# Optimization experiments

Measured on AMD Instinct MI355X. Metric: run time of the kernel, lower is better.

The kernel has to match this reference:

```python
import jax, jax.numpy as jnp
import numpy as np

V = 5023          # FLAME vertex count
NJ = 5            # joints: global, neck, jaw, eyeL, eyeR
N_SHAPE = 100
N_EXP = 50
PARENTS = np.array([-1, 0, 1, 1, 1], dtype=np.int64)  # static kintree
N_BATCH = 2048


def setup_inputs() -> dict:
    key = jax.random.key(0)
    ks = jax.random.split(key, 12)
    N = N_BATCH
    shape = jax.random.normal(ks[0], (N, N_SHAPE), jnp.float32)
    exp = jax.random.normal(ks[1], (N, N_EXP), jnp.float32)
    neck_pose = 0.1 * jax.random.normal(ks[2], (N, 3), jnp.float32)
    jaw_pose = 0.1 * jax.random.normal(ks[3], (N, 3), jnp.float32)
    eye_pose = 0.1 * jax.random.normal(ks[4], (N, 6), jnp.float32)
    v_template = jax.random.normal(ks[5], (V, 3), jnp.float32)
    shapedirs = 0.01 * jax.random.normal(ks[6], (V, 3, N_SHAPE + N_EXP), jnp.float32)
    posedirs = 0.01 * jax.random.normal(ks[7], (36, V * 3), jnp.float32)
    J_regressor = jax.random.uniform(ks[8], (NJ, V), jnp.float32)
    J_regressor = J_regressor / J_regressor.sum(axis=1, keepdims=True)
    lbs_weights = jax.random.uniform(ks[9], (V, NJ), jnp.float32)
    lbs_weights = lbs_weights / lbs_weights.sum(axis=1, keepdims=True)
    parents = jnp.asarray(PARENTS)
    return dict(shape=shape, exp=exp, neck_pose=neck_pose, jaw_pose=jaw_pose,
                eye_pose=eye_pose, v_template=v_template, shapedirs=shapedirs,
                posedirs=posedirs, J_regressor=J_regressor, lbs_weights=lbs_weights,
                parents=parents)


def rodrigues(rot_vecs):
    """Axis-angle [...,3] -> rotation matrices [...,3,3] (matches SMPL/FLAME impl)."""
    angle = jnp.linalg.norm(rot_vecs + 1e-8, axis=-1, keepdims=True)
    rd = rot_vecs / angle
    cos = jnp.cos(angle)[..., None]
    sin = jnp.sin(angle)[..., None]
    rx, ry, rz = rd[..., 0], rd[..., 1], rd[..., 2]
    z = jnp.zeros_like(rx)
    K = jnp.stack([z, -rz, ry, rz, z, -rx, -ry, rx, z], axis=-1).reshape(rd.shape + (3,))
    I = jnp.eye(3, dtype=rot_vecs.dtype)
    return I + sin * K + (1.0 - cos) * (K @ K)


def flame_forward(shape, exp, neck_pose, jaw_pose, eye_pose, v_template,
                  shapedirs, posedirs, J_regressor, lbs_weights):
    N = shape.shape[0]
    dt = shape.dtype
    betas = jnp.concatenate([shape, exp], axis=1)                      # [N,150]
    # full pose: zeroed global rot + neck + jaw + eyes -> [N,NJ,3]
    full_pose = jnp.concatenate([jnp.zeros_like(jaw_pose), neck_pose,
                                 jaw_pose, eye_pose], axis=1).reshape(N, NJ, 3)
    # shape blendshapes
    v_shaped = v_template[None] + jnp.einsum('bl,vkl->bvk', betas, shapedirs)  # [N,V,3]
    J = jnp.einsum('jv,bvk->bjk', J_regressor, v_shaped)               # [N,NJ,3]
    # pose blendshapes
    R = rodrigues(full_pose)                                           # [N,NJ,3,3]
    pose_feature = (R[:, 1:] - jnp.eye(3, dtype=dt)).reshape(N, (NJ - 1) * 9)
    v_posed = v_shaped + (pose_feature @ posedirs).reshape(N, V, 3)
    # kinematic chain (static 5-joint tree)
    rel_J = J.at[:, 1:].add(-J[:, PARENTS[1:]])
    Rt = jnp.concatenate([R, rel_J[..., None]], axis=-1)               # [N,NJ,3,4]
    bottom = jnp.broadcast_to(jnp.array([0., 0., 0., 1.], dtype=dt), (N, NJ, 1, 4))
    T = jnp.concatenate([Rt, bottom], axis=2)                          # [N,NJ,4,4]
    chain = [T[:, 0]]
    for i in range(1, NJ):
        chain.append(chain[int(PARENTS[i])] @ T[:, i])
    G = jnp.stack(chain, axis=1)                                       # [N,NJ,4,4]
    # remove rest-pose joint locations from the transforms
    J_h = jnp.concatenate([J, jnp.zeros((N, NJ, 1), dt)], axis=-1)     # [N,NJ,4]
    t_corr = jnp.einsum('bjrc,bjc->bjr', G, J_h)
    A = G.at[..., 3].add(-t_corr)                                      # [N,NJ,4,4]
    # linear blend skinning
    Tw = jnp.einsum('vj,bjrc->bvrc', lbs_weights, A)                   # [N,V,4,4]
    v_h = jnp.concatenate([v_posed, jnp.ones((N, V, 1), dt)], axis=-1)
    verts = jnp.einsum('bvrc,bvc->bvr', Tw, v_h)[..., :3]              # [N,V,3]
    return verts


def reference(shape, exp, neck_pose, jaw_pose, eye_pose, v_template,
              shapedirs, posedirs, J_regressor, lbs_weights, parents):
    # parents is a static buffer (PARENTS) -- accepted for signature parity.
    return flame_forward(shape, exp, neck_pose, jaw_pose, eye_pose, v_template,
                         shapedirs, posedirs, J_regressor, lbs_weights)
```

## Files before the change

kernel.cpp:

```cpp
#include <hip/hip_runtime.h>
#include <hip/hip_bf16.h>
#include <math.h>

#define NV   5023
#define N3   15069
#define NB   2048
#define NTIL 79
#define NPAD (NTIL*192)

#define WS_JD_B   0
#define WS_ATR_B  9216
#define WS_AB_B   795648
#define WS_BB_B   1582080

#define GP_J 126
#define GP_S 1067
#define GP_P 237

typedef __attribute__((ext_vector_type(8))) short short8;
typedef __attribute__((ext_vector_type(4))) float floatx4;

static __device__ __forceinline__ unsigned short f2bf(float x) {
    union { __hip_bfloat16 h; unsigned short s; } u;
    u.h = __float2bfloat16(x);
    return u.s;
}
static __device__ __forceinline__ unsigned int pk2(float a, float b) {
    return (unsigned int)f2bf(a) | ((unsigned int)f2bf(b) << 16);
}

#define BAR_LGKM() do { \
    asm volatile("s_waitcnt lgkmcnt(0)" ::: "memory"); \
    __builtin_amdgcn_s_barrier(); \
    asm volatile("" ::: "memory"); \
} while (0)

__global__ void k_prep(const float* __restrict__ Jreg,
                       const float* __restrict__ sdirs,
                       const float* __restrict__ vt,
                       const float* __restrict__ pdirs,
                       char* __restrict__ ws) {
    __shared__ float JregL[200];
    __shared__ float PL[36][65];
    const int t = threadIdx.x;

    if (blockIdx.x < GP_J) {
        int slice = blockIdx.x;
        int start = slice * 40;
        int end   = min(start + 40, NV);
        if (t < 200) {
            int j = t / 40, vl = t % 40;
            int v = start + vl;
            JregL[t] = (v < NV) ? Jreg[j * NV + v] : 0.f;
        }
        __syncthreads();
        int s0 = t, s1 = t + 256;
        float a0[5] = {0,0,0,0,0}, a1[5] = {0,0,0,0,0};
        #pragma unroll 2
        for (int v = start; v < end; ++v) {
            int vl = v - start;
            float x0 = (s0 < 450) ? sdirs[(size_t)v * 450 + s0]
                     : (s0 < 453 ? vt[v * 3 + (s0 - 450)] : 0.f);
            float x1 = (s1 < 450) ? sdirs[(size_t)v * 450 + s1]
                     : (s1 < 453 ? vt[v * 3 + (s1 - 450)] : 0.f);
            #pragma unroll
            for (int j = 0; j < 5; ++j) {
                float w = JregL[j * 40 + vl];
                a0[j] += w * x0; a1[j] += w * x1;
            }
        }
        float* Jd = (float*)(ws + WS_JD_B);
        #pragma unroll
        for (int j = 0; j < 5; ++j) {
            if (s0 < 453) atomicAdd(&Jd[j * 453 + s0], a0[j]);
            if (s1 < 453) atomicAdd(&Jd[j * 453 + s1], a1[j]);
        }
    } else if (blockIdx.x < GP_J + GP_S) {
        int idx = (blockIdx.x - GP_J) * 256 + t;
        if (idx < NPAD * 18) {
            int n = idx / 18, g = idx % 18;
            __hip_bfloat16* dst = (__hip_bfloat16*)(ws + WS_BB_B) + (size_t)n * 192 + g * 8;
            if (n < N3) {
                const float* src = sdirs + (size_t)n * 150 + g * 8;
                float2 p0 = *(const float2*)(src);
                float2 p1 = *(const float2*)(src + 2);
                float2 p2 = *(const float2*)(src + 4);
                float2 p3 = *(const float2*)(src + 6);
                unsigned int w[4] = { pk2(p0.x, p0.y), pk2(p1.x, p1.y),
                                      pk2(p2.x, p2.y), pk2(p3.x, p3.y) };
                *(int4*)dst = *(int4*)w;
            } else {
                int4 z = {0, 0, 0, 0};
                *(int4*)dst = z;
            }
        }
    } else {
        int pb = blockIdx.x - (GP_J + GP_S);
        int n0 = pb * 64;
        #pragma unroll
        for (int j = 0; j < 9; ++j) {
            int flat = j * 256 + t;
            int k = flat >> 6, i = flat & 63;
            int n = n0 + i;
            PL[k][i] = (n < N3) ? pdirs[(size_t)k * N3 + n] : 0.f;
        }
        __syncthreads();
        #pragma unroll
        for (int j = 0; j < 2; ++j) {
            int idx2 = j * 256 + t;
            if (idx2 < 384) {
                int r = idx2 / 6, g = idx2 % 6;
                int n = n0 + r;
                int k0 = 144 + g * 8;
                __hip_bfloat16 val[8];
                #pragma unroll
                for (int e = 0; e < 8; ++e) {
                    int k = k0 + e;
                    float v = 0.f;
                    if (k < 150)      v = (n < N3) ? sdirs[(size_t)n * 150 + k] : 0.f;
                    else if (k < 186) v = PL[k - 150][r];
                    val[e] = __float2bfloat16(v);
                }
                *(int4*)((__hip_bfloat16*)(ws + WS_BB_B) + (size_t)n * 192 + k0) = *(int4*)val;
            }
        }
    }
}

__global__ void k_batch(const float* __restrict__ shp,
                        const float* __restrict__ expn,
                        const float* __restrict__ neck,
                        const float* __restrict__ jaw,
                        const float* __restrict__ eye,
                        char* __restrict__ ws) {
    __shared__ float JdL[2265];
    {
        const float* Jd = (const float*)(ws + WS_JD_B);
        for (int i = threadIdx.x; i < 2265; i += 64) JdL[i] = Jd[i];
    }
    __syncthreads();
    int b = blockIdx.x * 64 + threadIdx.x;
    float* Atr = (float*)(ws + WS_ATR_B) + (size_t)b * 60;
    unsigned int* A32 = (unsigned int*)((char*)ws + WS_AB_B + (size_t)b * 384);

    float J[15];
    #pragma unroll
    for (int jk = 0; jk < 15; ++jk) J[jk] = JdL[(jk / 3) * 453 + 450 + (jk % 3)];

    for (int l4 = 0; l4 < 25; ++l4) {
        float4 be = *(const float4*)(shp + (size_t)b * 100 + l4 * 4);
        A32[2*l4]     = pk2(be.x, be.y);
        A32[2*l4 + 1] = pk2(be.z, be.w);
        float bev[4] = {be.x, be.y, be.z, be.w};
        #pragma unroll
        for (int e = 0; e < 4; ++e) {
            int l = l4 * 4 + e;
            #pragma unroll
            for (int jj = 0; jj < 5; ++jj)
                #pragma unroll
                for (int kk = 0; kk < 3; ++kk)
                    J[jj * 3 + kk] += JdL[jj * 453 + kk * 150 + l] * bev[e];
        }
    }
    for (int l2 = 0; l2 < 25; ++l2) {
        float2 be = *(const float2*)(expn + (size_t)b * 50 + l2 * 2);
        A32[50 + l2] = pk2(be.x, be.y);
        float bev[2] = {be.x, be.y};
        #pragma unroll
        for (int e = 0; e < 2; ++e) {
            int l = 100 + l2 * 2 + e;
            #pragma unroll
            for (int jj = 0; jj < 5; ++jj)
                #pragma unroll
                for (int kk = 0; kk < 3; ++kk)
                    J[jj * 3 + kk] += JdL[jj * 453 + kk * 150 + l] * bev[e];
        }
    }

    float R[5][9];
    for (int jj = 0; jj < 5; ++jj) {
        float rx, ry, rz;
        if (jj == 0)      { rx = 0.f; ry = 0.f; rz = 0.f; }
        else if (jj == 1) { rx = neck[b*3]; ry = neck[b*3+1]; rz = neck[b*3+2]; }
        else if (jj == 2) { rx = jaw[b*3];  ry = jaw[b*3+1];  rz = jaw[b*3+2];  }
        else if (jj == 3) { rx = eye[b*6];  ry = eye[b*6+1];  rz = eye[b*6+2];  }
        else              { rx = eye[b*6+3]; ry = eye[b*6+4]; rz = eye[b*6+5];  }
        float ax = rx + 1e-8f, ay = ry + 1e-8f, az = rz + 1e-8f;
        float angle = sqrtf(ax*ax + ay*ay + az*az);
        float inv = 1.f / angle;
        float ux = rx * inv, uy = ry * inv, uz = rz * inv;
        float c = cosf(angle), s = sinf(angle);
        float K[9] = {0.f, -uz, uy,  uz, 0.f, -ux,  -uy, ux, 0.f};
        float KK[9];
        #pragma unroll
        for (int r = 0; r < 3; ++r)
            #pragma unroll
            for (int cc = 0; cc < 3; ++cc) {
                float a = 0.f;
                #pragma unroll
                for (int m = 0; m < 3; ++m) a += K[r*3+m] * K[m*3+cc];
                KK[r*3+cc] = a;
            }
        #pragma unroll
        for (int e = 0; e < 9; ++e) R[jj][e] = s * K[e] + (1.f - c) * KK[e];
        R[jj][0] += 1.f; R[jj][4] += 1.f; R[jj][8] += 1.f;
    }

    float pf_loc[36];
    #pragma unroll
    for (int jj = 1; jj < 5; ++jj)
        #pragma unroll
        for (int e = 0; e < 9; ++e)
            pf_loc[(jj-1)*9 + e] = R[jj][e] - ((e == 0 || e == 4 || e == 8) ? 1.f : 0.f);
    #pragma unroll
    for (int i = 0; i < 18; ++i) A32[75 + i] = pk2(pf_loc[2*i], pf_loc[2*i + 1]);
    A32[93] = 0u; A32[94] = 0u; A32[95] = 0u;

    float G[5][12];
    #pragma unroll
    for (int r = 0; r < 3; ++r) {
        #pragma unroll
        for (int cc = 0; cc < 3; ++cc) G[0][r*4+cc] = R[0][r*3+cc];
        G[0][r*4+3] = J[r];
    }
    const int par[5] = {-1, 0, 1, 1, 1};
    for (int jj = 1; jj < 5; ++jj) {
        int p = par[jj];
        float rel[3];
        #pragma unroll
        for (int r = 0; r < 3; ++r) rel[r] = J[jj*3+r] - J[p*3+r];
        #pragma unroll
        for (int r = 0; r < 3; ++r) {
            #pragma unroll
            for (int cc = 0; cc < 3; ++cc) {
                float a = 0.f;
                #pragma unroll
                for (int m = 0; m < 3; ++m) a += G[p][r*4+m] * R[jj][m*3+cc];
                G[jj][r*4+cc] = a;
            }
            float tt = G[p][r*4+3];
            #pragma unroll
            for (int m = 0; m < 3; ++m) tt += G[p][r*4+m] * rel[m];
            G[jj][r*4+3] = tt;
        }
    }
    for (int jj = 0; jj < 5; ++jj)
        #pragma unroll
        for (int r = 0; r < 3; ++r) {
            float tc = 0.f;
            #pragma unroll
            for (int m = 0; m < 3; ++m) tc += G[jj][r*4+m] * J[jj*3+m];
            Atr[jj*12 + r*4 + 0] = G[jj][r*4+0];
            Atr[jj*12 + r*4 + 1] = G[jj][r*4+1];
            Atr[jj*12 + r*4 + 2] = G[jj][r*4+2];
            Atr[jj*12 + r*4 + 3] = G[jj][r*4+3] - tc;
        }
}

#define A_OFF  0
#define B_OFF  8704
#define S_VT   33
#define S_AT   61
#define VT_T_OFF 0
#define ATR_OFF  25344
#define VTQ_OFF  33152
#define LBS_OFF  33920
#define SMEM_BYTES 35200

__global__ __launch_bounds__(256, 3) void k_mega(
        const char* __restrict__ ws,
        const float* __restrict__ vt,
        const float* __restrict__ lbsw,
        float* __restrict__ out) {
    __shared__ __align__(16) unsigned char smem[SMEM_BYTES];
    const unsigned char* AbG = (const unsigned char*)ws + WS_AB_B;
    const unsigned char* BbG = (const unsigned char*)ws + WS_BB_B;
    const float* AtrG = (const float*)(ws + WS_ATR_B);

    const int ntile = blockIdx.y;
    const int b0    = blockIdx.x * 64;
    const int t     = threadIdx.x;
    const int lane  = t & 63;
    const int wn    = t >> 6;
    const int l15 = lane & 15, quad = lane >> 4;

    floatx4 acc[4][3];
    #pragma unroll
    for (int f = 0; f < 4; ++f)
        #pragma unroll
        for (int g = 0; g < 3; ++g) {
            floatx4 z = {0.f, 0.f, 0.f, 0.f};
            acc[f][g] = z;
        }

    for (int chunk = 0; chunk < 3; ++chunk) {
        __syncthreads();
        #pragma unroll
        for (int i = 0; i < 2; ++i) {
            int flat = i * 256 + t;
            int row = flat >> 3, piece = flat & 7;
            *(float4*)(smem + A_OFF + row * 136 + piece * 16) =
                *(const float4*)(AbG + (size_t)(b0 + row) * 384 + chunk * 128 + piece * 16);
        }
        #pragma unroll
        for (int i = 0; i < 6; ++i) {
            int flat = i * 256 + t;
            int row = flat >> 3, piece = flat & 7;
            *(float4*)(smem + B_OFF + row * 136 + piece * 16) =
                *(const float4*)(BbG + (size_t)(ntile * 192 + row) * 384 + chunk * 128 + piece * 16);
        }
        __syncthreads();
        #pragma unroll
        for (int ks = 0; ks < 2; ++ks) {
            short8 af[4];
            #pragma unroll
            for (int f = 0; f < 4; ++f)
                af[f] = *(const short8*)(smem + A_OFF + (f * 16 + l15) * 136 + ks * 64 + quad * 16);
            #pragma unroll
            for (int g = 0; g < 3; ++g) {
                short8 bf = *(const short8*)(smem + B_OFF + (wn * 48 + g * 16 + l15) * 136 + ks * 64 + quad * 16);
                #pragma unroll
                for (int f = 0; f < 4; ++f)
                    acc[f][g] = __builtin_amdgcn_mfma_f32_16x16x32_bf16(af[f], bf, acc[f][g], 0, 0, 0);
            }
        }
    }
    __syncthreads();

    float* vtT  = (float*)(smem + VT_T_OFF);
    float* atrS = (float*)(smem + ATR_OFF);
    float* vtQ  = (float*)(smem + VTQ_OFF);
    float* lbsS = (float*)(smem + LBS_OFF);

    if (t < 192) { int n = ntile * 192 + t; vtQ[t] = (n < N3) ? vt[n] : 0.f; }
    for (int i = t; i < 320; i += 256) {
        int v = ntile * 64 + i / 5;
        lbsS[i] = (v < NV) ? lbsw[(size_t)v * 5 + (i % 5)] : 0.f;
    }

    #pragma unroll
    for (int q = 0; q < 2; ++q) {
        BAR_LGKM();
        #pragma unroll
        for (int ff2 = 0; ff2 < 2; ++ff2) {
            int f = q * 2 + ff2;
            #pragma unroll
            for (int g = 0; g < 3; ++g) {
                int col = wn * 48 + g * 16 + l15;
                int rl  = ff2 * 16 + quad * 4;
                #pragma unroll
                for (int r = 0; r < 4; ++r)
                    vtT[col * S_VT + rl + r] = acc[f][g][r];
            }
        }
        for (int i = t; i < 1920; i += 256) {
            int rw = i / 60, cw = i - rw * 60;
            atrS[rw * S_AT + cw] = AtrG[((size_t)(b0 + q * 32)) * 60 + i];
        }
        BAR_LGKM();

        {
            int rl = t & 31;
            int vgrp = t >> 5;
            float ar[60];
            #pragma unroll
            for (int i = 0; i < 60; ++i) ar[i] = atrS[rl * S_AT + i];
            #pragma unroll
            for (int vv = 0; vv < 8; ++vv) {
                int vloc = vgrp * 8 + vv;
                int c0 = vloc * 3;
                float w0 = lbsS[vloc*5+0], w1 = lbsS[vloc*5+1], w2 = lbsS[vloc*5+2],
                      w3 = lbsS[vloc*5+3], w4 = lbsS[vloc*5+4];
                float px = vtT[(c0+0) * S_VT + rl] + vtQ[c0+0];
                float py = vtT[(c0+1) * S_VT + rl] + vtQ[c0+1];
                float pz = vtT[(c0+2) * S_VT + rl] + vtQ[c0+2];
                float y[3];
                #pragma unroll
                for (int r = 0; r < 3; ++r) {
                    float t0 = w0*ar[ 0+r*4+0] + w1*ar[12+r*4+0] + w2*ar[24+r*4+0]
                             + w3*ar[36+r*4+0] + w4*ar[48+r*4+0];
                    float t1 = w0*ar[ 0+r*4+1] + w1*ar[12+r*4+1] + w2*ar[24+r*4+1]
                             + w3*ar[36+r*4+1] + w4*ar[48+r*4+1];
                    float t2 = w0*ar[ 0+r*4+2] + w1*ar[12+r*4+2] + w2*ar[24+r*4+2]
                             + w3*ar[36+r*4+2] + w4*ar[48+r*4+2];
                    float t3 = w0*ar[ 0+r*4+3] + w1*ar[12+r*4+3] + w2*ar[24+r*4+3]
                             + w3*ar[36+r*4+3] + w4*ar[48+r*4+3];
                    y[r] = t0*px + t1*py + t2*pz + t3;
                }
                vtT[(c0+0) * S_VT + rl] = y[0];
                vtT[(c0+1) * S_VT + rl] = y[1];
                vtT[(c0+2) * S_VT + rl] = y[2];
            }
        }
        BAR_LGKM();
        {
            int wv = t >> 6;
            const bool full = (ntile * 192 + 192 <= N3);
            for (int rr = wv; rr < 32; rr += 4) {
                size_t ob = (size_t)(b0 + q * 32 + rr) * N3 + (size_t)ntile * 192;
                if (full) {
                    #pragma unroll
                    for (int e = 0; e < 3; ++e) {
                        int col = e * 64 + lane;
                        __builtin_nontemporal_store(vtT[col * S_VT + rr], &out[ob + col]);
                    }
                } else {
                    #pragma unroll
                    for (int e = 0; e < 3; ++e) {
                        int col = e * 64 + lane;
                        if (ntile * 192 + col < N3)
                            __builtin_nontemporal_store(vtT[col * S_VT + rr], &out[ob + col]);
                    }
                }
            }
        }
    }
}

extern "C" void kernel_launch(void* const* d_in, const int* in_sizes, int n_in,
                              void* d_out, int out_size, void* d_ws, size_t ws_size,
                              hipStream_t stream) {
    const float* shp  = (const float*)d_in[0];
    const float* expn = (const float*)d_in[1];
    const float* neck = (const float*)d_in[2];
    const float* jaw  = (const float*)d_in[3];
    const float* eye  = (const float*)d_in[4];
    const float* vt   = (const float*)d_in[5];
    const float* sdir = (const float*)d_in[6];
    const float* pdir = (const float*)d_in[7];
    const float* jreg = (const float*)d_in[8];
    const float* lbsw = (const float*)d_in[9];
    char* ws  = (char*)d_ws;
    float* out = (float*)d_out;

    hipMemsetAsync(ws + WS_JD_B, 0, 2272 * 4, stream);
    k_prep <<<GP_J + GP_S + GP_P, 256, 0, stream>>>(jreg, sdir, vt, pdir, ws);
    k_batch<<<32, 64, 0, stream>>>(shp, expn, neck, jaw, eye, ws);
    k_mega <<<dim3(32, NTIL), 256, 0, stream>>>(ws, vt, lbsw, out);
}
```

Measured before the change: 255.5 us.

## Specialize batch kernel for zero global pose and prefetch Atr into registers

The per-batch kernel now skips the Rodrigues computation for the always-zero global joint, treating its transform as identity. It also expands the kinematic chain explicitly for the static parent tree. In the main kernel, each phase's 32x60 Atr block is loaded from global memory into registers ahead of use, with the second block fetched during the first phase, so the global-load latency overlaps other work. Output stores change from nontemporal to ordinary stores, which may alter cache behaviour for the large output write.

```diff
diff --git a/kernel.cpp b/kernel.cpp
--- a/kernel.cpp
+++ b/kernel.cpp
@@ -127,6 +127,28 @@
     }
 }
 
+static __device__ __forceinline__ void rodr3(float rx, float ry, float rz, float* R) {
+    float ax = rx + 1e-8f, ay = ry + 1e-8f, az = rz + 1e-8f;
+    float angle = sqrtf(ax*ax + ay*ay + az*az);
+    float inv = 1.f / angle;
+    float ux = rx * inv, uy = ry * inv, uz = rz * inv;
+    float c = cosf(angle), s = sinf(angle);
+    float K[9] = {0.f, -uz, uy,  uz, 0.f, -ux,  -uy, ux, 0.f};
+    float KK[9];
+    #pragma unroll
+    for (int r = 0; r < 3; ++r)
+        #pragma unroll
+        for (int cc = 0; cc < 3; ++cc) {
+            float a = 0.f;
+            #pragma unroll
+            for (int m = 0; m < 3; ++m) a += K[r*3+m] * K[m*3+cc];
+            KK[r*3+cc] = a;
+        }
+    #pragma unroll
+    for (int e = 0; e < 9; ++e) R[e] = s * K[e] + (1.f - c) * KK[e];
+    R[0] += 1.f; R[4] += 1.f; R[8] += 1.f;
+}
+
 __global__ void k_batch(const float* __restrict__ shp,
                         const float* __restrict__ expn,
                         const float* __restrict__ neck,
@@ -177,84 +199,59 @@
         }
     }
 
-    float R[5][9];
-    for (int jj = 0; jj < 5; ++jj) {
-        float rx, ry, rz;
-        if (jj == 0)      { rx = 0.f; ry = 0.f; rz = 0.f; }
-        else if (jj == 1) { rx = neck[b*3]; ry = neck[b*3+1]; rz = neck[b*3+2]; }
-        else if (jj == 2) { rx = jaw[b*3];  ry = jaw[b*3+1];  rz = jaw[b*3+2];  }
-        else if (jj == 3) { rx = eye[b*6];  ry = eye[b*6+1];  rz = eye[b*6+2];  }
-        else              { rx = eye[b*6+3]; ry = eye[b*6+4]; rz = eye[b*6+5];  }
-        float ax = rx + 1e-8f, ay = ry + 1e-8f, az = rz + 1e-8f;
-        float angle = sqrtf(ax*ax + ay*ay + az*az);
-        float inv = 1.f / angle;
-        float ux = rx * inv, uy = ry * inv, uz = rz * inv;
-        float c = cosf(angle), s = sinf(angle);
-        float K[9] = {0.f, -uz, uy,  uz, 0.f, -ux,  -uy, ux, 0.f};
-        float KK[9];
-        #pragma unroll
-        for (int r = 0; r < 3; ++r)
+    float R[4][9];
+    rodr3(neck[b*3], neck[b*3+1], neck[b*3+2], R[0]);
+    rodr3(jaw[b*3],  jaw[b*3+1],  jaw[b*3+2],  R[1]);
+    rodr3(eye[b*6],  eye[b*6+1],  eye[b*6+2],  R[2]);
+    rodr3(eye[b*6+3], eye[b*6+4], eye[b*6+5],  R[3]);
+
+    #pragma unroll
+    for (int i = 0; i < 18; ++i) {
+        int x0 = 2*i, x1 = 2*i + 1;
+        float p0 = R[x0/9][x0%9] - (((x0%9) % 4) == 0 ? 1.f : 0.f);
+        float p1 = R[x1/9][x1%9] - (((x1%9) % 4) == 0 ? 1.f : 0.f);
+        A32[75 + i] = pk2(p0, p1);
+    }
+    A32[93] = 0u; A32[94] = 0u; A32[95] = 0u;
+
+    Atr[0]=1.f; Atr[1]=0.f; Atr[2]=0.f;  Atr[3]=0.f;
+    Atr[4]=0.f; Atr[5]=1.f; Atr[6]=0.f;  Atr[7]=0.f;
+    Atr[8]=0.f; Atr[9]=0.f; Atr[10]=1.f; Atr[11]=0.f;
+    #pragma unroll
+    for (int r = 0; r < 3; ++r) {
+        float d = R[0][r*3+0]*J[3] + R[0][r*3+1]*J[4] + R[0][r*3+2]*J[5];
+        Atr[12 + r*4 + 0] = R[0][r*3+0];
+        Atr[12 + r*4 + 1] = R[0][r*3+1];
+        Atr[12 + r*4 + 2] = R[0][r*3+2];
+        Atr[12 + r*4 + 3] = J[3+r] - d;
+    }
+    #pragma unroll
+    for (int kk = 1; kk < 4; ++kk) {
+        int jj = kk + 1;
+        float rel[3];
+        #pragma unroll
+        for (int r = 0; r < 3; ++r) rel[r] = J[jj*3+r] - J[3+r];
+        float Gr[9], tv[3];
+        #pragma unroll
+        for (int r = 0; r < 3; ++r) {
             #pragma unroll
             for (int cc = 0; cc < 3; ++cc) {
                 float a = 0.f;
                 #pragma unroll
-                for (int m = 0; m < 3; ++m) a += K[r*3+m] * K[m*3+cc];
-                KK[r*3+cc] = a;
+                for (int m = 0; m < 3; ++m) a += R[0][r*3+m] * R[kk][m*3+cc];
+                Gr[r*3+cc] = a;
             }
-        #pragma unroll
-        for (int e = 0; e < 9; ++e) R[jj][e] = s * K[e] + (1.f - c) * KK[e];
-        R[jj][0] += 1.f; R[jj][4] += 1.f; R[jj][8] += 1.f;
-    }
-
-    float pf_loc[36];
-    #pragma unroll
-    for (int jj = 1; jj < 5; ++jj)
-        #pragma unroll
-        for (int e = 0; e < 9; ++e)
-            pf_loc[(jj-1)*9 + e] = R[jj][e] - ((e == 0 || e == 4 || e == 8) ? 1.f : 0.f);
-    #pragma unroll
-    for (int i = 0; i < 18; ++i) A32[75 + i] = pk2(pf_loc[2*i], pf_loc[2*i + 1]);
-    A32[93] = 0u; A32[94] = 0u; A32[95] = 0u;
-
-    float G[5][12];
-    #pragma unroll
-    for (int r = 0; r < 3; ++r) {
-        #pragma unroll
-        for (int cc = 0; cc < 3; ++cc) G[0][r*4+cc] = R[0][r*3+cc];
-        G[0][r*4+3] = J[r];
-    }
-    const int par[5] = {-1, 0, 1, 1, 1};
-    for (int jj = 1; jj < 5; ++jj) {
-        int p = par[jj];
-        float rel[3];
-        #pragma unroll
-        for (int r = 0; r < 3; ++r) rel[r] = J[jj*3+r] - J[p*3+r];
+            tv[r] = R[0][r*3+0]*rel[0] + R[0][r*3+1]*rel[1] + R[0][r*3+2]*rel[2] + J[3+r];
+        }
         #pragma unroll
         for (int r = 0; r < 3; ++r) {
-            #pragma unroll
-            for (int cc = 0; cc < 3; ++cc) {
-                float a = 0.f;
-                #pragma unroll
-                for (int m = 0; m < 3; ++m) a += G[p][r*4+m] * R[jj][m*3+cc];
-                G[jj][r*4+cc] = a;
-            }
-            float tt = G[p][r*4+3];
-            #pragma unroll
-            for (int m = 0; m < 3; ++m) tt += G[p][r*4+m] * rel[m];
-            G[jj][r*4+3] = tt;
-        }
-    }
-    for (int jj = 0; jj < 5; ++jj)
-        #pragma unroll
-        for (int r = 0; r < 3; ++r) {
-            float tc = 0.f;
-            #pragma unroll
-            for (int m = 0; m < 3; ++m) tc += G[jj][r*4+m] * J[jj*3+m];
-            Atr[jj*12 + r*4 + 0] = G[jj][r*4+0];
-            Atr[jj*12 + r*4 + 1] = G[jj][r*4+1];
-            Atr[jj*12 + r*4 + 2] = G[jj][r*4+2];
-            Atr[jj*12 + r*4 + 3] = G[jj][r*4+3] - tc;
-        }
+            float d = Gr[r*3+0]*J[jj*3+0] + Gr[r*3+1]*J[jj*3+1] + Gr[r*3+2]*J[jj*3+2];
+            Atr[jj*12 + r*4 + 0] = Gr[r*3+0];
+            Atr[jj*12 + r*4 + 1] = Gr[r*3+1];
+            Atr[jj*12 + r*4 + 2] = Gr[r*3+2];
+            Atr[jj*12 + r*4 + 3] = tv[r] - d;
+        }
+    }
 }
 
 #define A_OFF  0
@@ -337,84 +334,107 @@
         int v = ntile * 64 + i / 5;
         lbsS[i] = (v < NV) ? lbsw[(size_t)v * 5 + (i % 5)] : 0.f;
     }
-
-    #pragma unroll
-    for (int q = 0; q < 2; ++q) {
-        BAR_LGKM();
-        #pragma unroll
-        for (int ff2 = 0; ff2 < 2; ++ff2) {
-            int f = q * 2 + ff2;
-            #pragma unroll
-            for (int g = 0; g < 3; ++g) {
-                int col = wn * 48 + g * 16 + l15;
-                int rl  = ff2 * 16 + quad * 4;
-                #pragma unroll
-                for (int r = 0; r < 4; ++r)
-                    vtT[col * S_VT + rl + r] = acc[f][g][r];
-            }
-        }
-        for (int i = t; i < 1920; i += 256) {
-            int rw = i / 60, cw = i - rw * 60;
-            atrS[rw * S_AT + cw] = AtrG[((size_t)(b0 + q * 32)) * 60 + i];
-        }
-        BAR_LGKM();
-
-        {
-            int rl = t & 31;
-            int vgrp = t >> 5;
-            float ar[60];
-            #pragma unroll
-            for (int i = 0; i < 60; ++i) ar[i] = atrS[rl * S_AT + i];
-            #pragma unroll
-            for (int vv = 0; vv < 8; ++vv) {
-                int vloc = vgrp * 8 + vv;
-                int c0 = vloc * 3;
-                float w0 = lbsS[vloc*5+0], w1 = lbsS[vloc*5+1], w2 = lbsS[vloc*5+2],
-                      w3 = lbsS[vloc*5+3], w4 = lbsS[vloc*5+4];
-                float px = vtT[(c0+0) * S_VT + rl] + vtQ[c0+0];
-                float py = vtT[(c0+1) * S_VT + rl] + vtQ[c0+1];
-                float pz = vtT[(c0+2) * S_VT + rl] + vtQ[c0+2];
-                float y[3];
-                #pragma unroll
-                for (int r = 0; r < 3; ++r) {
-                    float t0 = w0*ar[ 0+r*4+0] + w1*ar[12+r*4+0] + w2*ar[24+r*4+0]
-                             + w3*ar[36+r*4+0] + w4*ar[48+r*4+0];
-                    float t1 = w0*ar[ 0+r*4+1] + w1*ar[12+r*4+1] + w2*ar[24+r*4+1]
-                             + w3*ar[36+r*4+1] + w4*ar[48+r*4+1];
-                    float t2 = w0*ar[ 0+r*4+2] + w1*ar[12+r*4+2] + w2*ar[24+r*4+2]
-                             + w3*ar[36+r*4+2] + w4*ar[48+r*4+2];
-                    float t3 = w0*ar[ 0+r*4+3] + w1*ar[12+r*4+3] + w2*ar[24+r*4+3]
-                             + w3*ar[36+r*4+3] + w4*ar[48+r*4+3];
-                    y[r] = t0*px + t1*py + t2*pz + t3;
-                }
-                vtT[(c0+0) * S_VT + rl] = y[0];
-                vtT[(c0+1) * S_VT + rl] = y[1];
-                vtT[(c0+2) * S_VT + rl] = y[2];
-            }
-        }
-        BAR_LGKM();
-        {
-            int wv = t >> 6;
-            const bool full = (ntile * 192 + 192 <= N3);
-            for (int rr = wv; rr < 32; rr += 4) {
-                size_t ob = (size_t)(b0 + q * 32 + rr) * N3 + (size_t)ntile * 192;
-                if (full) {
-                    #pragma unroll
-                    for (int e = 0; e < 3; ++e) {
-                        int col = e * 64 + lane;
-                        __builtin_nontemporal_store(vtT[col * S_VT + rr], &out[ob + col]);
-                    }
-                } else {
-                    #pragma unroll
-                    for (int e = 0; e < 3; ++e) {
-                        int col = e * 64 + lane;
-                        if (ntile * 192 + col < N3)
-                            __builtin_nontemporal_store(vtT[col * S_VT + rr], &out[ob + col]);
-                    }
-                }
-            }
-        }
-    }
+    float arA[8], arB[8];
+    #pragma unroll
+    for (int u = 0; u < 8; ++u) {
+        int i = u * 256 + t;
+        arA[u] = (i < 1920) ? AtrG[(size_t)b0 * 60 + i] : 0.f;
+    }
+
+    #define EPI_PHASE(QQ, ARCUR, PRELOAD_NEXT)                                          \
+    {                                                                                   \
+        BAR_LGKM();                                                                     \
+                                   \
+        _Pragma("unroll")                                                               \
+        for (int ff2 = 0; ff2 < 2; ++ff2) {                                             \
+            int f = QQ * 2 + ff2;                                                       \
+            _Pragma("unroll")                                                           \
+            for (int g = 0; g < 3; ++g) {                                               \
+                int col = wn * 48 + g * 16 + l15;                                       \
+                int rl  = ff2 * 16 + quad * 4;                                          \
+                _Pragma("unroll")                                                       \
+                for (int r = 0; r < 4; ++r)                                             \
+                    vtT[col * S_VT + rl + r] = acc[f][g][r];                            \
+            }                                                                           \
+        }                                                                               \
+                                                         \
+        _Pragma("unroll")                                                               \
+        for (int u = 0; u < 8; ++u) {                                                   \
+            int i = u * 256 + t;                                                        \
+            if (i < 1920) {                                                             \
+                int rw = i / 60, cw = i - rw * 60;                                      \
+                atrS[rw * S_AT + cw] = ARCUR[u];                                        \
+            }                                                                           \
+        }                                                                               \
+        PRELOAD_NEXT                                                                    \
+        BAR_LGKM();                                                                     \
+                                        \
+        {                                                                               \
+            int rl = t & 31;                                                            \
+            int vgrp = t >> 5;                                                          \
+            float ar[60];                                                               \
+            _Pragma("unroll")                                                           \
+            for (int i = 0; i < 60; ++i) ar[i] = atrS[rl * S_AT + i];                   \
+            _Pragma("unroll")                                                           \
+            for (int vv = 0; vv < 8; ++vv) {                                            \
+                int vloc = vgrp * 8 + vv;                                               \
+                int c0 = vloc * 3;                                                      \
+                float w0 = lbsS[vloc*5+0], w1 = lbsS[vloc*5+1], w2 = lbsS[vloc*5+2],    \
+                      w3 = lbsS[vloc*5+3], w4 = lbsS[vloc*5+4];                         \
+                float px = vtT[(c0+0) * S_VT + rl] + vtQ[c0+0];                         \
+                float py = vtT[(c0+1) * S_VT + rl] + vtQ[c0+1];                         \
+                float pz = vtT[(c0+2) * S_VT + rl] + vtQ[c0+2];                         \
+                float y[3];                                                             \
+                _Pragma("unroll")                                                       \
+                for (int r = 0; r < 3; ++r) {                                           \
+                    float t0 = w0*ar[ 0+r*4+0] + w1*ar[12+r*4+0] + w2*ar[24+r*4+0]      \
+                             + w3*ar[36+r*4+0] + w4*ar[48+r*4+0];                       \
+                    float t1 = w0*ar[ 0+r*4+1] + w1*ar[12+r*4+1] + w2*ar[24+r*4+1]      \
+                             + w3*ar[36+r*4+1] + w4*ar[48+r*4+1];                       \
+                    float t2 = w0*ar[ 0+r*4+2] + w1*ar[12+r*4+2] + w2*ar[24+r*4+2]      \
+                             + w3*ar[36+r*4+2] + w4*ar[48+r*4+2];                       \
+                    float t3 = w0*ar[ 0+r*4+3] + w1*ar[12+r*4+3] + w2*ar[24+r*4+3]      \
+                             + w3*ar[36+r*4+3] + w4*ar[48+r*4+3];                       \
+                    y[r] = t0*px + t1*py + t2*pz + t3;                                  \
+                }                                                                       \
+                vtT[(c0+0) * S_VT + rl] = y[0];                                         \
+                vtT[(c0+1) * S_VT + rl] = y[1];                                         \
+                vtT[(c0+2) * S_VT + rl] = y[2];                                         \
+            }                                                                           \
+        }                                                                               \
+        BAR_LGKM();                                                                     \
+                  \
+        {                                                                               \
+            int wv = t >> 6;                                                            \
+            const bool full = (ntile * 192 + 192 <= N3);                                \
+            for (int rr = wv; rr < 32; rr += 4) {                                       \
+                size_t ob = (size_t)(b0 + QQ * 32 + rr) * N3 + (size_t)ntile * 192;     \
+                if (full) {                                                             \
+                    _Pragma("unroll")                                                   \
+                    for (int e = 0; e < 3; ++e) {                                       \
+                        int col = e * 64 + lane;                                        \
+                        out[ob + col] = vtT[col * S_VT + rr];                           \
+                    }                                                                   \
+                } else {                                                                \
+                    _Pragma("unroll")                                                   \
+                    for (int e = 0; e < 3; ++e) {                                       \
+                        int col = e * 64 + lane;                                        \
+                        if (ntile * 192 + col < N3)                                     \
+                            out[ob + col] = vtT[col * S_VT + rr];                       \
+                    }                                                                   \
+                }                                                                       \
+            }                                                                           \
+        }                                                                               \
+    }
+
+    EPI_PHASE(0, arA,
+        { _Pragma("unroll")
+          for (int u = 0; u < 8; ++u) {
+              int i = u * 256 + t;
+              arB[u] = (i < 1920) ? AtrG[(size_t)(b0 + 32) * 60 + i] : 0.f;
+          } } )
+    EPI_PHASE(1, arB, { } )
+    #undef EPI_PHASE
 }
 
 extern "C" void kernel_launch(void* const* d_in, const int* in_sizes, int n_in,
```

After: 247.6 us. -3.1%, faster.
